# Performance work log

Hardware: AMD Instinct MI355X
Metric: run time of the kernel (lower is better)

The kernel has to match this reference:

```python
import jax, jax.numpy as jnp
import numpy as np

_N = 512
_L = 65536


def setup_inputs() -> dict:
    key = jax.random.key(0)
    ks = jax.random.split(key, 11)
    N, L = _N, _L
    sc = 1.0 / np.sqrt(N)  # lecun-normal style scaling
    f = lambda k, s: jax.random.normal(k, s, dtype=jnp.float32)
    return {
        # stable DPLR spectrum: negative real parts
        "Lambda_re": -(jax.random.uniform(ks[0], (N,), dtype=jnp.float32) + 0.1),
        "Lambda_im": f(ks[1], (N,)),
        "p_re": f(ks[2], (N,)), "p_im": f(ks[3], (N,)),
        "q_re": f(ks[4], (N,)), "q_im": f(ks[5], (N,)),
        "Vc_re": f(ks[6], (N, N)) * sc, "Vc_im": f(ks[7], (N, N)) * sc,
        "Ct": f(ks[8], (1, N, 2)) * sc,
        "B": f(ks[9], (N, 1)) * sc,
        "log_step": jax.random.uniform(ks[10], (1,), dtype=jnp.float32)
                    * (np.log(0.1) - np.log(0.001)) + np.log(0.001),
        "L": L,
    }


def reference(Lambda_re, Lambda_im, p_re, p_im, q_re, q_im,
              Vc_re, Vc_im, Ct, B, log_step, L):
    Lambda = Lambda_re + 1j * Lambda_im            # (N,)
    p = p_re + 1j * p_im                           # (N,)
    q = q_re + 1j * q_im                           # (N,)
    Vc = Vc_re + 1j * Vc_im                        # (N,N)
    Ct_c = Ct[..., 0] + 1j * Ct[..., 1]            # (1,N)
    Bc = (Vc @ B.astype(Vc.dtype)).ravel()         # (N,) complex, B = Vc @ B
    step = jnp.exp(log_step)[0]

    # aterm = (Ct*, q*), bterm = (B, p)
    a0 = Ct_c.conj().ravel()
    a1 = q.conj()
    b0 = Bc
    b1 = p

    # roots of unity
    Omega = jnp.exp(-2j * jnp.pi * (jnp.arange(L) / L))   # (L,)
    g = (2.0 / step) * ((1.0 - Omega) / (1.0 + Omega))    # (L,) bilinear transform
    c = 2.0 / (1.0 + Omega)                               # (L,)

    # single fused Cauchy pass: resolvent (L,N) contracted with all 4 rank-1 terms
    r = 1.0 / (g[:, None] - Lambda[None, :])               # (L,N)
    terms = jnp.stack([a0 * b0, a0 * b1, a1 * b0, a1 * b1], axis=1)  # (N,4)
    K = r @ terms                                          # (L,4): k00,k01,k10,k11
    k00, k01, k10, k11 = K[:, 0], K[:, 1], K[:, 2], K[:, 3]

    atRoots = c * (k00 - k01 * (1.0 / (1.0 + k11)) * k10)  # Woodbury correction
    out = jnp.fft.ifft(atRoots, L).reshape(L)
    return out.real
```

## Files before the change

kernel.cpp:

```cpp
#include <hip/hip_runtime.h>
#include <math.h>

constexpr int WS_TERMS = 0;
constexpr int WS_ZT    = 8192;

__device__ __forceinline__ float sin2pi(float x) { return __builtin_amdgcn_sinf(x); }
__device__ __forceinline__ float cos2pi(float x) { return __builtin_amdgcn_cosf(x); }

__global__ __launch_bounds__(256) void k_setup(
    const float* __restrict__ Lr, const float* __restrict__ Li,
    const float* __restrict__ pr, const float* __restrict__ pi,
    const float* __restrict__ qr, const float* __restrict__ qi,
    const float* __restrict__ Vr, const float* __restrict__ Vi,
    const float* __restrict__ Ct, const float* __restrict__ Bv,
    const float* __restrict__ log_step,
    float* __restrict__ terms)
{
    __shared__ float red[8];
    int n = blockIdx.x;
    int t = threadIdx.x;
    float b0 = Bv[t], b1 = Bv[t + 256];
    float sr = fmaf(Vr[n*512 + t], b0, Vr[n*512 + t + 256] * b1);
    float si = fmaf(Vi[n*512 + t], b0, Vi[n*512 + t + 256] * b1);
    #pragma unroll
    for (int off = 32; off > 0; off >>= 1) {
        sr += __shfl_down(sr, off, 64);
        si += __shfl_down(si, off, 64);
    }
    if ((t & 63) == 0) { red[(t >> 6)*2] = sr; red[(t >> 6)*2 + 1] = si; }
    __syncthreads();
    if (t == 0) {
        float b0r = red[0] + red[2] + red[4] + red[6];
        float b0i = red[1] + red[3] + red[5] + red[7];
        double step = exp((double)log_step[0]);
        float t2s = (float)(2.0 / step);
        float lr  = Lr[n];
        float a0r = Ct[2*n], a0i = -Ct[2*n+1];
        float a1r = qr[n],   a1i = -qi[n];
        float b1r = pr[n],   b1i = pi[n];
        float* tm = terms + n * 12;
        tm[0]  = -lr;                 tm[1]  = Li[n];
        tm[2]  = a0r*b0r - a0i*b0i;   tm[3]  = a0r*b0i + a0i*b0r;
        tm[4]  = a0r*b1r - a0i*b1i;   tm[5]  = a0r*b1i + a0i*b1r;
        tm[6]  = a1r*b0r - a1i*b0i;   tm[7]  = a1r*b0i + a1i*b0r;
        tm[8]  = a1r*b1r - a1i*b1i;   tm[9]  = a1r*b1i + a1i*b1r;
        tm[10] = lr*lr;               tm[11] = t2s;
    }
}

__global__ __launch_bounds__(512, 8) void k_mainA(
    const float* __restrict__ terms,
    float* __restrict__ ZTf)
{
    __shared__ float buf[6144];
    int tid = threadIdx.x;
    int b   = blockIdx.x;
    int l1      = b >> 2;
    int quarter = b & 3;

    {
        float4* dst = (float4*)buf;
        const float4* src = (const float4*)terms;
        #pragma unroll
        for (int i = 0; i < 3; ++i) dst[tid + 512*i] = src[tid + 512*i];
    }

    int u     = tid & 63;
    int chunk = tid >> 6;
    int l2    = quarter*64 + u;
    int l     = l1 + 256*l2;

    float tv2 = (float)l * (1.0f / 131072.0f);
    float sn  = sin2pi(tv2), cn = cos2pi(tv2);
    float T   = sn / cn;
    __syncthreads();
    float t2s = buf[11];
    float g_i = t2s * T;
    if (!(fabsf(T) <= 1.0e6f)) { g_i = 3e30f; T = 0.f; }

    float ac[8];
    #pragma unroll
    for (int c = 0; c < 8; ++c) ac[c] = 0.f;

    const float4* t4 = (const float4*)buf + chunk * 64 * 3;
    #pragma unroll 4
    for (int n = 0; n < 64; ++n) {
        float4 Aq = t4[n*3 + 0];
        float4 Bq = t4[n*3 + 1];
        float4 Cq = t4[n*3 + 2];
        float di = g_i - Aq.y;
        float dd = fmaf(di, di, Cq.z);
        float iv = __builtin_amdgcn_rcpf(dd);
        float rr = Aq.x * iv;
        float ri = -di * iv;
        ac[0] = fmaf(rr, Aq.z, ac[0]); ac[0] = fmaf(-ri, Aq.w, ac[0]);
        ac[1] = fmaf(rr, Aq.w, ac[1]); ac[1] = fmaf( ri, Aq.z, ac[1]);
        ac[2] = fmaf(rr, Bq.x, ac[2]); ac[2] = fmaf(-ri, Bq.y, ac[2]);
        ac[3] = fmaf(rr, Bq.y, ac[3]); ac[3] = fmaf( ri, Bq.x, ac[3]);
        ac[4] = fmaf(rr, Bq.z, ac[4]); ac[4] = fmaf(-ri, Bq.w, ac[4]);
        ac[5] = fmaf(rr, Bq.w, ac[5]); ac[5] = fmaf( ri, Bq.z, ac[5]);
        ac[6] = fmaf(rr, Cq.x, ac[6]); ac[6] = fmaf(-ri, Cq.y, ac[6]);
        ac[7] = fmaf(rr, Cq.y, ac[7]); ac[7] = fmaf( ri, Cq.x, ac[7]);
    }
    __syncthreads();

    if (chunk >= 4) {
        float* p = buf + (chunk - 4) * 576 + u * 9;
        #pragma unroll
        for (int c = 0; c < 8; ++c) p[c] = ac[c];
    }
    __syncthreads();
    if (chunk < 4) {
        float* p = buf + chunk * 576 + u * 9;
        #pragma unroll
        for (int c = 0; c < 8; ++c) p[c] += ac[c];
    }
    __syncthreads();

    {
        int a = (tid >> 3) * 9 + (tid & 7);
        buf[2304 + a] = buf[a] + buf[576 + a] + buf[1152 + a] + buf[1728 + a];
    }
    __syncthreads();

    if (tid < 64) {
        const float* rd = buf + 2304 + tid * 9;
        float s0r = rd[0], s0i = rd[1], s1r = rd[2], s1i = rd[3];
        float s2r = rd[4], s2i = rd[5], s3r = rd[6], s3i = rd[7];
        float e1r = 1.f + s3r, e1i = s3i;
        float eiv = 1.0f / fmaf(e1r, e1r, e1i * e1i);
        float m_r = s1r * s2r - s1i * s2i;
        float m_i = s1r * s2i + s1i * s2r;
        float q_r = (m_r * e1r + m_i * e1i) * eiv;
        float q_i = (m_i * e1r - m_r * e1i) * eiv;
        float u_r = s0r - q_r;
        float u_i = s0i - q_i;
        ((float2*)buf)[tid] = make_float2(u_r - T * u_i, u_i + T * u_r);
    }
    __syncthreads();

    {
        int t1 = tid & 255;
        int s  = tid >> 8;
        int j0 = s * 32;
        int mm0 = ((quarter*64 + j0) * t1) & 255;
        float curR = cos2pi((float)mm0 * (1.0f/256.0f));
        float curI = sin2pi((float)mm0 * (1.0f/256.0f));
        float rotR = cos2pi((float)t1 * (1.0f/256.0f));
        float rotI = sin2pi((float)t1 * (1.0f/256.0f));
        const float2* xrow = (const float2*)buf;
        float yr = 0.f, yi = 0.f;
        #pragma unroll 8
        for (int j = j0; j < j0 + 32; ++j) {
            float2 x = xrow[j];
            yr = fmaf(x.x, curR, yr); yr = fmaf(-x.y, curI, yr);
            yi = fmaf(x.x, curI, yi); yi = fmaf( x.y, curR, yi);
            float nR = curR * rotR - curI * rotI;
            float nI = curR * rotI + curI * rotR;
            curR = nR; curI = nI;
        }
        ((float2*)(buf + 128))[tid] = make_float2(yr, yi);
    }
    __syncthreads();
    if (tid < 256) {
        const float2* pA = (const float2*)(buf + 128);
        float2 p0 = pA[tid], p1 = pA[tid + 256];
        float Yr = p0.x + p1.x;
        float Yi = p0.y + p1.y;
        int mm = (l1 * tid) & 65535;
        float tv = (float)mm * (1.0f / 65536.0f);
        float twR = cos2pi(tv), twI = sin2pi(tv);
        ((float2*)(ZTf + quarter * 131072))[tid * 256 + l1] =
            make_float2(Yr * twR - Yi * twI, Yr * twI + Yi * twR);
    }
}

__global__ __launch_bounds__(256) void k_fftB(
    const float* __restrict__ ZTf, float* __restrict__ out)
{
    __shared__ float buf2[768];
    int tid = threadIdx.x;
    int b   = blockIdx.x;
    int t1 = b >> 2;
    int qT = b & 3;
    {
        float2 z = make_float2(0.f, 0.f);
        #pragma unroll
        for (int q = 0; q < 4; ++q) {
            float2 v = ((const float2*)(ZTf + q * 131072))[t1 * 256 + tid];
            z.x += v.x; z.y += v.y;
        }
        ((float2*)buf2)[tid] = z;
    }
    int k2 = tid & 63;
    int s  = tid >> 6;
    int t2 = qT * 64 + k2;
    int m0 = (s * t2) & 3;
    float curR = (m0 == 0) ? 1.f : (m0 == 2 ? -1.f : 0.f);
    float curI = (m0 == 1) ? 1.f : (m0 == 3 ? -1.f : 0.f);
    float rotR = cos2pi((float)t2 * (1.0f / 256.0f));
    float rotI = sin2pi((float)t2 * (1.0f / 256.0f));
    __syncthreads();
    const float2* zrow = (const float2*)buf2;
    float o = 0.f;
    #pragma unroll 8
    for (int j = s * 64; j < s * 64 + 64; ++j) {
        float2 z = zrow[j];
        o = fmaf(z.x, curR, o);
        o = fmaf(-z.y, curI, o);
        float nR = curR * rotR - curI * rotI;
        float nI = curR * rotI + curI * rotR;
        curR = nR; curI = nI;
    }
    buf2[512 + tid] = o;
    __syncthreads();
    if (tid < 64) {
        float sum = buf2[512+tid] + buf2[512+tid+64] + buf2[512+tid+128] + buf2[512+tid+192];
        out[t1 + 256 * (qT * 64 + tid)] = sum * (1.0f / 65536.0f);
    }
}

extern "C" void kernel_launch(void* const* d_in, const int* in_sizes, int n_in,
                              void* d_out, int out_size, void* d_ws, size_t ws_size,
                              hipStream_t stream)
{
    const float* Lambda_re = (const float*)d_in[0];
    const float* Lambda_im = (const float*)d_in[1];
    const float* p_re      = (const float*)d_in[2];
    const float* p_im      = (const float*)d_in[3];
    const float* q_re      = (const float*)d_in[4];
    const float* q_im      = (const float*)d_in[5];
    const float* Vc_re     = (const float*)d_in[6];
    const float* Vc_im     = (const float*)d_in[7];
    const float* Ct        = (const float*)d_in[8];
    const float* Bv        = (const float*)d_in[9];
    const float* log_step  = (const float*)d_in[10];

    float* wsf   = (float*)d_ws;
    float* terms = wsf + WS_TERMS;
    float* ZT    = wsf + WS_ZT;
    float* outp  = (float*)d_out;

    k_setup<<<512, 256, 0, stream>>>(Lambda_re, Lambda_im, p_re, p_im, q_re, q_im,
                                     Vc_re, Vc_im, Ct, Bv, log_step, terms);
    k_mainA<<<1024, 512, 0, stream>>>(terms, ZT);
    k_fftB<<<1024, 256, 0, stream>>>(ZT, outp);
}
```

Baseline: 105.7 us.

## Process four frequency quarters per block to reuse LDS loads and drop partial sums

```diff
diff --git a/kernel.cpp b/kernel.cpp
--- a/kernel.cpp
+++ b/kernel.cpp
@@ -48,15 +48,13 @@
     }
 }
 
-__global__ __launch_bounds__(512, 8) void k_mainA(
+__global__ __launch_bounds__(512) void k_mainA(
     const float* __restrict__ terms,
     float* __restrict__ ZTf)
 {
-    __shared__ float buf[6144];
+    __shared__ float buf[9024];
     int tid = threadIdx.x;
-    int b   = blockIdx.x;
-    int l1      = b >> 2;
-    int quarter = b & 3;
+    int l1  = blockIdx.x;
 
     {
         float4* dst = (float4*)buf;
@@ -67,111 +65,130 @@
 
     int u     = tid & 63;
     int chunk = tid >> 6;
-    int l2    = quarter*64 + u;
-    int l     = l1 + 256*l2;
-
-    float tv2 = (float)l * (1.0f / 131072.0f);
-    float sn  = sin2pi(tv2), cn = cos2pi(tv2);
-    float T   = sn / cn;
-    __syncthreads();
-    float t2s = buf[11];
-    float g_i = t2s * T;
-    if (!(fabsf(T) <= 1.0e6f)) { g_i = 3e30f; T = 0.f; }
-
-    float ac[8];
-    #pragma unroll
-    for (int c = 0; c < 8; ++c) ac[c] = 0.f;
+
+    float t2s = terms[11];
+
+    float T[4], g_i[4];
+    #pragma unroll
+    for (int q = 0; q < 4; ++q) {
+        int l = l1 + 256*(u + 64*q);
+        float tv2 = (float)l * (1.0f / 131072.0f);
+        float sn  = sin2pi(tv2), cn = cos2pi(tv2);
+        float Tq  = sn / cn;
+        float gq  = t2s * Tq;
+        if (!(fabsf(Tq) <= 1.0e6f)) { gq = 3e30f; Tq = 0.f; }
+        T[q] = Tq; g_i[q] = gq;
+    }
+    __syncthreads();
+
+    float ac[4][8];
+    #pragma unroll
+    for (int q = 0; q < 4; ++q)
+        #pragma unroll
+        for (int c = 0; c < 8; ++c) ac[q][c] = 0.f;
 
     const float4* t4 = (const float4*)buf + chunk * 64 * 3;
-    #pragma unroll 4
+    #pragma unroll 2
     for (int n = 0; n < 64; ++n) {
         float4 Aq = t4[n*3 + 0];
         float4 Bq = t4[n*3 + 1];
         float4 Cq = t4[n*3 + 2];
-        float di = g_i - Aq.y;
-        float dd = fmaf(di, di, Cq.z);
-        float iv = __builtin_amdgcn_rcpf(dd);
-        float rr = Aq.x * iv;
-        float ri = -di * iv;
-        ac[0] = fmaf(rr, Aq.z, ac[0]); ac[0] = fmaf(-ri, Aq.w, ac[0]);
-        ac[1] = fmaf(rr, Aq.w, ac[1]); ac[1] = fmaf( ri, Aq.z, ac[1]);
-        ac[2] = fmaf(rr, Bq.x, ac[2]); ac[2] = fmaf(-ri, Bq.y, ac[2]);
-        ac[3] = fmaf(rr, Bq.y, ac[3]); ac[3] = fmaf( ri, Bq.x, ac[3]);
-        ac[4] = fmaf(rr, Bq.z, ac[4]); ac[4] = fmaf(-ri, Bq.w, ac[4]);
-        ac[5] = fmaf(rr, Bq.w, ac[5]); ac[5] = fmaf( ri, Bq.z, ac[5]);
-        ac[6] = fmaf(rr, Cq.x, ac[6]); ac[6] = fmaf(-ri, Cq.y, ac[6]);
-        ac[7] = fmaf(rr, Cq.y, ac[7]); ac[7] = fmaf( ri, Cq.x, ac[7]);
-    }
-    __syncthreads();
-
-    if (chunk >= 4) {
-        float* p = buf + (chunk - 4) * 576 + u * 9;
         #pragma unroll
-        for (int c = 0; c < 8; ++c) p[c] = ac[c];
-    }
-    __syncthreads();
-    if (chunk < 4) {
-        float* p = buf + chunk * 576 + u * 9;
-        #pragma unroll
-        for (int c = 0; c < 8; ++c) p[c] += ac[c];
-    }
-    __syncthreads();
-
-    {
-        int a = (tid >> 3) * 9 + (tid & 7);
-        buf[2304 + a] = buf[a] + buf[576 + a] + buf[1152 + a] + buf[1728 + a];
-    }
-    __syncthreads();
-
-    if (tid < 64) {
-        const float* rd = buf + 2304 + tid * 9;
-        float s0r = rd[0], s0i = rd[1], s1r = rd[2], s1i = rd[3];
-        float s2r = rd[4], s2i = rd[5], s3r = rd[6], s3i = rd[7];
-        float e1r = 1.f + s3r, e1i = s3i;
-        float eiv = 1.0f / fmaf(e1r, e1r, e1i * e1i);
-        float m_r = s1r * s2r - s1i * s2i;
-        float m_i = s1r * s2i + s1i * s2r;
-        float q_r = (m_r * e1r + m_i * e1i) * eiv;
-        float q_i = (m_i * e1r - m_r * e1i) * eiv;
-        float u_r = s0r - q_r;
-        float u_i = s0i - q_i;
-        ((float2*)buf)[tid] = make_float2(u_r - T * u_i, u_i + T * u_r);
-    }
-    __syncthreads();
-
-    {
-        int t1 = tid & 255;
-        int s  = tid >> 8;
-        int j0 = s * 32;
-        int mm0 = ((quarter*64 + j0) * t1) & 255;
-        float curR = cos2pi((float)mm0 * (1.0f/256.0f));
-        float curI = sin2pi((float)mm0 * (1.0f/256.0f));
-        float rotR = cos2pi((float)t1 * (1.0f/256.0f));
-        float rotI = sin2pi((float)t1 * (1.0f/256.0f));
-        const float2* xrow = (const float2*)buf;
-        float yr = 0.f, yi = 0.f;
-        #pragma unroll 8
-        for (int j = j0; j < j0 + 32; ++j) {
-            float2 x = xrow[j];
-            yr = fmaf(x.x, curR, yr); yr = fmaf(-x.y, curI, yr);
-            yi = fmaf(x.x, curI, yi); yi = fmaf( x.y, curR, yi);
-            float nR = curR * rotR - curI * rotI;
-            float nI = curR * rotI + curI * rotR;
-            curR = nR; curI = nI;
-        }
-        ((float2*)(buf + 128))[tid] = make_float2(yr, yi);
-    }
-    __syncthreads();
+        for (int q = 0; q < 4; ++q) {
+            float di = g_i[q] - Aq.y;
+            float dd = fmaf(di, di, Cq.z);
+            float iv = __builtin_amdgcn_rcpf(dd);
+            float rr = Aq.x * iv;
+            float ri = -di * iv;
+            ac[q][0] = fmaf(rr, Aq.z, ac[q][0]); ac[q][0] = fmaf(-ri, Aq.w, ac[q][0]);
+            ac[q][1] = fmaf(rr, Aq.w, ac[q][1]); ac[q][1] = fmaf( ri, Aq.z, ac[q][1]);
+            ac[q][2] = fmaf(rr, Bq.x, ac[q][2]); ac[q][2] = fmaf(-ri, Bq.y, ac[q][2]);
+            ac[q][3] = fmaf(rr, Bq.y, ac[q][3]); ac[q][3] = fmaf( ri, Bq.x, ac[q][3]);
+            ac[q][4] = fmaf(rr, Bq.z, ac[q][4]); ac[q][4] = fmaf(-ri, Bq.w, ac[q][4]);
+            ac[q][5] = fmaf(rr, Bq.w, ac[q][5]); ac[q][5] = fmaf( ri, Bq.z, ac[q][5]);
+            ac[q][6] = fmaf(rr, Cq.x, ac[q][6]); ac[q][6] = fmaf(-ri, Cq.y, ac[q][6]);
+            ac[q][7] = fmaf(rr, Cq.y, ac[q][7]); ac[q][7] = fmaf( ri, Cq.x, ac[q][7]);
+        }
+    }
+    __syncthreads();
+
+    float accR = 0.f, accI = 0.f;
+
+    #pragma unroll
+    for (int q = 0; q < 4; ++q) {
+        if (chunk >= 4) {
+            float* p = buf + 6144 + (chunk - 4) * 576 + u * 9;
+            #pragma unroll
+            for (int c = 0; c < 8; ++c) p[c] = ac[q][c];
+        }
+        __syncthreads();
+        if (chunk < 4) {
+            float* p = buf + 6144 + chunk * 576 + u * 9;
+            #pragma unroll
+            for (int c = 0; c < 8; ++c) p[c] += ac[q][c];
+        }
+        __syncthreads();
+
+        {
+            int a = (tid >> 3) * 9 + (tid & 7);
+            buf[8448 + a] = buf[6144 + a] + buf[6720 + a] + buf[7296 + a] + buf[7872 + a];
+        }
+        __syncthreads();
+
+        if (tid < 64) {
+            const float* rd = buf + 8448 + tid * 9;
+            float s0r = rd[0], s0i = rd[1], s1r = rd[2], s1i = rd[3];
+            float s2r = rd[4], s2i = rd[5], s3r = rd[6], s3i = rd[7];
+            float e1r = 1.f + s3r, e1i = s3i;
+            float eiv = 1.0f / fmaf(e1r, e1r, e1i * e1i);
+            float m_r = s1r * s2r - s1i * s2i;
+            float m_i = s1r * s2i + s1i * s2r;
+            float q_r = (m_r * e1r + m_i * e1i) * eiv;
+            float q_i = (m_i * e1r - m_r * e1i) * eiv;
+            float u_r = s0r - q_r;
+            float u_i = s0i - q_i;
+            float Tq  = T[q];
+            ((float2*)buf)[tid] = make_float2(u_r - Tq * u_i, u_i + Tq * u_r);
+        }
+        __syncthreads();
+
+        {
+            int t1 = tid & 255;
+            int s  = tid >> 8;
+            int j0 = s * 32;
+            int mm0 = ((q*64 + j0) * t1) & 255;
+            float curR = cos2pi((float)mm0 * (1.0f/256.0f));
+            float curI = sin2pi((float)mm0 * (1.0f/256.0f));
+            float rotR = cos2pi((float)t1 * (1.0f/256.0f));
+            float rotI = sin2pi((float)t1 * (1.0f/256.0f));
+            const float2* xrow = (const float2*)buf;
+            float yr = 0.f, yi = 0.f;
+            #pragma unroll 8
+            for (int j = j0; j < j0 + 32; ++j) {
+                float2 x = xrow[j];
+                yr = fmaf(x.x, curR, yr); yr = fmaf(-x.y, curI, yr);
+                yi = fmaf(x.x, curI, yi); yi = fmaf( x.y, curR, yi);
+                float nR = curR * rotR - curI * rotI;
+                float nI = curR * rotI + curI * rotR;
+                curR = nR; curI = nI;
+            }
+            ((float2*)(buf + 128))[tid] = make_float2(yr, yi);
+        }
+        __syncthreads();
+        if (tid < 256) {
+            const float2* pA = (const float2*)(buf + 128);
+            float2 p0 = pA[tid], p1 = pA[tid + 256];
+            accR += p0.x + p1.x;
+            accI += p0.y + p1.y;
+        }
+    }
+
     if (tid < 256) {
-        const float2* pA = (const float2*)(buf + 128);
-        float2 p0 = pA[tid], p1 = pA[tid + 256];
-        float Yr = p0.x + p1.x;
-        float Yi = p0.y + p1.y;
         int mm = (l1 * tid) & 65535;
         float tv = (float)mm * (1.0f / 65536.0f);
         float twR = cos2pi(tv), twI = sin2pi(tv);
-        ((float2*)(ZTf + quarter * 131072))[tid * 256 + l1] =
-            make_float2(Yr * twR - Yi * twI, Yr * twI + Yi * twR);
+        ((float2*)ZTf)[tid * 256 + l1] =
+            make_float2(accR * twR - accI * twI, accR * twI + accI * twR);
     }
 }
 
@@ -184,13 +201,8 @@
     int t1 = b >> 2;
     int qT = b & 3;
     {
-        float2 z = make_float2(0.f, 0.f);
-        #pragma unroll
-        for (int q = 0; q < 4; ++q) {
-            float2 v = ((const float2*)(ZTf + q * 131072))[t1 * 256 + tid];
-            z.x += v.x; z.y += v.y;
-        }
-        ((float2*)buf2)[tid] = z;
+        float2 v = ((const float2*)ZTf)[t1 * 256 + tid];
+        ((float2*)buf2)[tid] = v;
     }
     int k2 = tid & 63;
     int s  = tid >> 6;
@@ -243,6 +255,6 @@
 
     k_setup<<<512, 256, 0, stream>>>(Lambda_re, Lambda_im, p_re, p_im, q_re, q_im,
                                      Vc_re, Vc_im, Ct, Bv, log_step, terms);
-    k_mainA<<<1024, 512, 0, stream>>>(terms, ZT);
+    k_mainA<<<256, 512, 0, stream>>>(terms, ZT);
     k_fftB<<<1024, 256, 0, stream>>>(ZT, outp);
 }
```

Measured after the change: 108.1 us. 2.3% more time.
